# Kernel optimization log

Measured on AMD Instinct MI355X. Metric: run time of the kernel, lower is better.

Reference implementation:

```python
import jax, jax.numpy as jnp
import numpy as np

NUM_GROUPS = 17
NUM_OCCLUDED = 10
TEMP = 0.1


def setup_inputs() -> dict:
    key = jax.random.key(0)
    k1, k2 = jax.random.split(key)
    B, N, D = 128, 577, 768
    x = jax.random.normal(k1, (B, N, D), dtype=jnp.float32)
    # xavier_uniform-like scale for (D, G) weight
    bound = float(np.sqrt(6.0 / (D + NUM_GROUPS)))
    group_weights = jax.random.uniform(k2, (D, NUM_GROUPS), dtype=jnp.float32, minval=-bound, maxval=bound)
    return {"x": x, "group_weights": group_weights}


def _l2_normalize(v):
    # matches F.normalize(dim=-1, eps=1e-12)
    return v / jnp.maximum(jnp.linalg.norm(v, axis=-1, keepdims=True), 1e-12)


def reference(x, group_weights):
    B, N, D = x.shape
    cls_token = x[:, 0, :]            # (B, D)
    patch_tokens = x[:, 1:, :]        # (B, P, D), P = N-1

    # cosine similarity of each patch with cls token
    sim = jnp.einsum('bpd,bd->bp', _l2_normalize(patch_tokens), _l2_normalize(cls_token))  # (B, P)

    # k least-similar patches are "occluded" -> zero them out
    _, occ_idx = jax.lax.top_k(-sim, NUM_OCCLUDED)  # (B, K)
    mask = jnp.ones_like(sim).at[jnp.arange(B)[:, None], occ_idx].set(0.0)  # (B, P)
    non_occ = patch_tokens * mask[..., None]  # (B, P, D)

    # attention-style group pooling; softmax over groups (dim=1)
    scores = jnp.einsum('dg,bpd->bgp', group_weights, non_occ) / TEMP  # (B, G, P)
    attn = jax.nn.softmax(scores, axis=1)
    group_features = jnp.einsum('bgp,bpd->bgd', attn, non_occ)  # (B, G, D)

    # pack [global_feat, group_feat_1..G] as (B, 1+G, D)
    feats = jnp.concatenate([cls_token[:, None, :], group_features], axis=1)
    return feats, attn
```

## Files before the change

### kernel.cpp

```cpp
#include <hip/hip_runtime.h>
#include <math.h>

#define B_ 128
#define NTOK 577
#define P_ 576
#define D_ 768
#define G_ 17
#define KOCC 10
#define INV_TEMP 10.0f
#define U17 (1.0f / 17.0f)

#define OFF_WT 0
#define OFF_SIM (G_ * D_)
#define OFF_CLSINV (OFF_SIM + B_ * P_)
#define OFF_OCC (OFF_CLSINV + B_)
#define OFF_GFP (OFF_OCC + B_ * KOCC)
#define GFP_PART ((size_t)B_ * G_ * D_)

__global__ __launch_bounds__(256) void k0_cls(const float* __restrict__ x,
                                              const float* __restrict__ gw,
                                              float* __restrict__ feats,
                                              float* __restrict__ clsinv,
                                              float* __restrict__ wt,
                                              int zero_groups) {
    if (blockIdx.x >= B_) {
        int g = blockIdx.x - B_;
        for (int d = threadIdx.x; d < D_; d += 256)
            wt[g * D_ + d] = gw[d * G_ + g];
        return;
    }
    int b = blockIdx.x;
    const float* cls = x + (size_t)b * NTOK * D_;
    float* fb = feats + (size_t)b * 18 * D_;
    float ss = 0.f;
    for (int i = threadIdx.x; i < D_ / 4; i += 256) {
        float4 v = ((const float4*)cls)[i];
        ((float4*)fb)[i] = v;
        ss = fmaf(v.x, v.x, fmaf(v.y, v.y, fmaf(v.z, v.z, fmaf(v.w, v.w, ss))));
    }
    if (zero_groups) {
        float4 z = {0.f, 0.f, 0.f, 0.f};
        for (int i = threadIdx.x; i < G_ * D_ / 4; i += 256)
            ((float4*)(fb + D_))[i] = z;
    }
    #pragma unroll
    for (int off = 32; off; off >>= 1) ss += __shfl_xor(ss, off, 64);
    __shared__ float red[4];
    int wave = threadIdx.x >> 6, lane = threadIdx.x & 63;
    if (lane == 0) red[wave] = ss;
    __syncthreads();
    if (threadIdx.x == 0) {
        float t = red[0] + red[1] + red[2] + red[3];
        clsinv[b] = 1.0f / fmaxf(sqrtf(t), 1e-12f);
    }
}

__global__ __launch_bounds__(256) void k1_score(const float* __restrict__ x,
                                                const float* __restrict__ wt,
                                                const float* __restrict__ clsinv,
                                                float* __restrict__ sim,
                                                float* __restrict__ attn) {
    __shared__ __align__(16) float buf[2][18 * 64];
    __shared__ __align__(16) float atile[19 * 68];
    int tid = threadIdx.x;
    int b = blockIdx.y, chunk = blockIdx.x;
    const float* clsrow = x + (size_t)b * NTOK * D_;

    for (int i = tid; i < 288; i += 256) {
        int r = i >> 4, c = i & 15;
        const float* src = (r < 17) ? (wt + r * D_ + c * 4) : (clsrow + c * 4);
        *(float4*)&buf[0][r * 64 + c * 4] = *(const float4*)src;
    }
    int lane = tid & 63, wave = tid >> 6;
    int lr = lane & 15, row4 = lane >> 4;
    int pbase = wave * 16 + row4 * 4;
    const float* xp0 = x + ((size_t)(b * NTOK + 1 + chunk * 64 + pbase)) * D_ + lr * 4;

    float4 xv[4], xn[4];
    #pragma unroll
    for (int m = 0; m < 4; ++m) xv[m] = *(const float4*)(xp0 + (size_t)m * D_);

    float s[19][4];
    #pragma unroll
    for (int i = 0; i < 19; ++i)
        #pragma unroll
        for (int m = 0; m < 4; ++m) s[i][m] = 0.f;
    __syncthreads();

    for (int kc = 0; kc < 12; ++kc) {
        int cb = kc & 1, nb = cb ^ 1;
        if (kc < 11) {
            #pragma unroll
            for (int m = 0; m < 4; ++m)
                xn[m] = *(const float4*)(xp0 + (kc + 1) * 64 + (size_t)m * D_);
            for (int i = tid; i < 288; i += 256) {
                int r = i >> 4, c = i & 15;
                const float* src = (r < 17) ? (wt + r * D_ + (kc + 1) * 64 + c * 4)
                                            : (clsrow + (kc + 1) * 64 + c * 4);
                *(float4*)&buf[nb][r * 64 + c * 4] = *(const float4*)src;
            }
        }
        #pragma unroll
        for (int g = 0; g < 18; ++g) {
            float4 w4 = *(const float4*)&buf[cb][g * 64 + lr * 4];
            #pragma unroll
            for (int m = 0; m < 4; ++m)
                s[g][m] = fmaf(xv[m].x, w4.x, fmaf(xv[m].y, w4.y,
                          fmaf(xv[m].z, w4.z, fmaf(xv[m].w, w4.w, s[g][m]))));
        }
        #pragma unroll
        for (int m = 0; m < 4; ++m)
            s[18][m] = fmaf(xv[m].x, xv[m].x, fmaf(xv[m].y, xv[m].y,
                       fmaf(xv[m].z, xv[m].z, fmaf(xv[m].w, xv[m].w, s[18][m]))));
        #pragma unroll
        for (int m = 0; m < 4; ++m) xv[m] = xn[m];
        __syncthreads();
    }

    #pragma unroll
    for (int off = 8; off >= 1; off >>= 1)
        #pragma unroll
        for (int i = 0; i < 19; ++i)
            #pragma unroll
            for (int m = 0; m < 4; ++m)
                s[i][m] += __shfl_xor(s[i][m], off, 16);

    #pragma unroll
    for (int g = 0; g < 19; ++g) {
        if (lr == ((g < 16) ? g : 15)) {
            float4 v = {s[g][0], s[g][1], s[g][2], s[g][3]};
            *(float4*)&atile[g * 68 + pbase] = v;
        }
    }
    __syncthreads();

    if (tid < 64) {
        int p = chunk * 64 + tid;
        float v[17];
        float mx = -3.0e38f;
        #pragma unroll
        for (int g = 0; g < 17; ++g) {
            v[g] = atile[g * 68 + tid];
            mx = fmaxf(mx, v[g]);
        }
        float tot = 0.f;
        #pragma unroll
        for (int g = 0; g < 17; ++g) {
            v[g] = __expf((v[g] - mx) * INV_TEMP);
            tot += v[g];
        }
        float inv = 1.0f / tot;
        float* ap = attn + ((size_t)b * G_) * P_ + p;
        #pragma unroll
        for (int g = 0; g < 17; ++g) ap[(size_t)g * P_] = v[g] * inv;
        float cd = atile[17 * 68 + tid];
        float sq = atile[18 * 68 + tid];
        sim[(size_t)b * P_ + p] = cd * clsinv[b] / fmaxf(sqrtf(sq), 1e-12f);
    }
}

__global__ __launch_bounds__(64) void k2_occl(const float* __restrict__ sim,
                                              float* __restrict__ attn,
                                              int* __restrict__ occ_idx) {
    int b = blockIdx.x, lane = threadIdx.x;
    int base = lane * 9;
    float v[9];
    #pragma unroll
    for (int j = 0; j < 9; ++j) v[j] = sim[(size_t)b * P_ + base + j];
    int wins[KOCC];
    for (int t = 0; t < KOCC; ++t) {
        float mv = 3.0e38f;
        int mi = 1 << 30;
        #pragma unroll
        for (int j = 0; j < 9; ++j) {
            if (v[j] < mv) { mv = v[j]; mi = base + j; }
        }
        #pragma unroll
        for (int off = 1; off < 64; off <<= 1) {
            float ov = __shfl_xor(mv, off, 64);
            int oi = __shfl_xor(mi, off, 64);
            if (ov < mv || (ov == mv && oi < mi)) { mv = ov; mi = oi; }
        }
        wins[t] = mi;
        int loc = mi - base;
        if (loc >= 0 && loc < 9) v[loc] = 3.0e38f;
    }
    if (lane == 0) {
        #pragma unroll
        for (int t = 0; t < KOCC; ++t) occ_idx[b * KOCC + t] = wins[t];
    }
    #pragma unroll
    for (int t = 0; t < KOCC; ++t) {
        if (lane < G_) attn[((size_t)b * G_ + lane) * P_ + wins[t]] = U17;
    }
}

__global__ __launch_bounds__(192) void k3_part(const float* __restrict__ x,
                                               const float* __restrict__ attn,
                                               float* __restrict__ gfp,
                                               int ppp) {
    extern __shared__ float am[];
    int tid = threadIdx.x;
    int pc = blockIdx.x, b = blockIdx.y;
    int p0 = pc * ppp;

    for (int i = tid; i < G_ * ppp; i += 192) {
        int g = i / ppp;
        int pp = i - g * ppp;
        am[i] = attn[((size_t)b * G_ + g) * P_ + p0 + pp];
    }
    __syncthreads();

    const float* xb = x + ((size_t)(b * NTOK) + 1 + p0) * D_ + tid * 4;
    float4 acc[G_];
    #pragma unroll
    for (int g = 0; g < G_; ++g) acc[g] = make_float4(0.f, 0.f, 0.f, 0.f);

    float4 c0 = *(const float4*)(xb + (size_t)0 * D_);
    float4 c1 = *(const float4*)(xb + (size_t)1 * D_);
    float4 c2 = *(const float4*)(xb + (size_t)2 * D_);
    float4 c3 = *(const float4*)(xb + (size_t)3 * D_);

    for (int pp = 0; pp < ppp; pp += 4) {
        float4 n0, n1, n2, n3;
        if (pp + 4 < ppp) {
            n0 = *(const float4*)(xb + (size_t)(pp + 4) * D_);
            n1 = *(const float4*)(xb + (size_t)(pp + 5) * D_);
            n2 = *(const float4*)(xb + (size_t)(pp + 6) * D_);
            n3 = *(const float4*)(xb + (size_t)(pp + 7) * D_);
        }
        #pragma unroll
        for (int g = 0; g < G_; ++g) {
            float4 a = *(const float4*)&am[g * ppp + pp];
            acc[g].x = fmaf(a.x, c0.x, fmaf(a.y, c1.x, fmaf(a.z, c2.x, fmaf(a.w, c3.x, acc[g].x))));
            acc[g].y = fmaf(a.x, c0.y, fmaf(a.y, c1.y, fmaf(a.z, c2.y, fmaf(a.w, c3.y, acc[g].y))));
            acc[g].z = fmaf(a.x, c0.z, fmaf(a.y, c1.z, fmaf(a.z, c2.z, fmaf(a.w, c3.z, acc[g].z))));
            acc[g].w = fmaf(a.x, c0.w, fmaf(a.y, c1.w, fmaf(a.z, c2.w, fmaf(a.w, c3.w, acc[g].w))));
        }
        c0 = n0; c1 = n1; c2 = n2; c3 = n3;
    }

    float* gb = gfp + ((size_t)(pc * B_ + b) * G_) * D_ + tid * 4;
    #pragma unroll
    for (int g = 0; g < G_; ++g) *(float4*)(gb + (size_t)g * D_) = acc[g];
}

#define PC_ 96
__global__ __launch_bounds__(192) void k3_atomic(const float* __restrict__ x,
                                                 const float* __restrict__ attn,
                                                 float* __restrict__ feats) {
    __shared__ __align__(16) float am[G_ * PC_];
    int tid = threadIdx.x;
    int pc = blockIdx.x, b = blockIdx.y;
    int p0 = pc * PC_;
    for (int i = tid; i < G_ * PC_; i += 192) {
        int g = i / PC_;
        int pp = i - g * PC_;
        am[i] = attn[((size_t)b * G_ + g) * P_ + p0 + pp];
    }
    __syncthreads();
    const float* xb = x + ((size_t)(b * NTOK) + 1 + p0) * D_ + tid * 4;
    float4 acc[G_];
    #pragma unroll
    for (int g = 0; g < G_; ++g) acc[g] = make_float4(0.f, 0.f, 0.f, 0.f);
    for (int pp = 0; pp < PC_; pp += 4) {
        float4 x0 = *(const float4*)(xb + (size_t)(pp + 0) * D_);
        float4 x1 = *(const float4*)(xb + (size_t)(pp + 1) * D_);
        float4 x2 = *(const float4*)(xb + (size_t)(pp + 2) * D_);
        float4 x3 = *(const float4*)(xb + (size_t)(pp + 3) * D_);
        #pragma unroll
        for (int g = 0; g < G_; ++g) {
            float4 a = *(const float4*)&am[g * PC_ + pp];
            acc[g].x = fmaf(a.x, x0.x, fmaf(a.y, x1.x, fmaf(a.z, x2.x, fmaf(a.w, x3.x, acc[g].x))));
            acc[g].y = fmaf(a.x, x0.y, fmaf(a.y, x1.y, fmaf(a.z, x2.y, fmaf(a.w, x3.y, acc[g].y))));
            acc[g].z = fmaf(a.x, x0.z, fmaf(a.y, x1.z, fmaf(a.z, x2.z, fmaf(a.w, x3.z, acc[g].z))));
            acc[g].w = fmaf(a.x, x0.w, fmaf(a.y, x1.w, fmaf(a.z, x2.w, fmaf(a.w, x3.w, acc[g].w))));
        }
    }
    float* fb = feats + ((size_t)(b * 18) + 1) * D_ + tid * 4;
    #pragma unroll
    for (int g = 0; g < G_; ++g) {
        atomicAdd(fb + (size_t)g * D_ + 0, acc[g].x);
        atomicAdd(fb + (size_t)g * D_ + 1, acc[g].y);
        atomicAdd(fb + (size_t)g * D_ + 2, acc[g].z);
        atomicAdd(fb + (size_t)g * D_ + 3, acc[g].w);
    }
}

__global__ __launch_bounds__(192) void k4_fin(const float* __restrict__ x,
                                              const int* __restrict__ occ_idx,
                                              const float* __restrict__ gfp,
                                              int nparts,
                                              float* __restrict__ feats) {
    int b = blockIdx.x, tid = threadIdx.x;
    float* fb = feats + ((size_t)(b * 18) + 1) * D_ + tid * 4;
    float4 acc[G_];
    if (nparts == 0) {
        #pragma unroll
        for (int g = 0; g < G_; ++g) acc[g] = *(const float4*)(fb + (size_t)g * D_);
    } else {
        #pragma unroll
        for (int g = 0; g < G_; ++g) acc[g] = make_float4(0.f, 0.f, 0.f, 0.f);
        for (int pc = 0; pc < nparts; ++pc) {
            const float* gb = gfp + ((size_t)(pc * B_ + b) * G_) * D_ + tid * 4;
            #pragma unroll
            for (int g = 0; g < G_; ++g) {
                float4 v = *(const float4*)(gb + (size_t)g * D_);
                acc[g].x += v.x; acc[g].y += v.y; acc[g].z += v.z; acc[g].w += v.w;
            }
        }
    }
    float4 corr = make_float4(0.f, 0.f, 0.f, 0.f);
    for (int t = 0; t < KOCC; ++t) {
        int p = occ_idx[b * KOCC + t];
        float4 xo = *(const float4*)(x + ((size_t)(b * NTOK) + 1 + p) * D_ + tid * 4);
        corr.x += xo.x; corr.y += xo.y; corr.z += xo.z; corr.w += xo.w;
    }
    corr.x *= U17; corr.y *= U17; corr.z *= U17; corr.w *= U17;
    #pragma unroll
    for (int g = 0; g < G_; ++g) {
        float4 v = acc[g];
        v.x -= corr.x; v.y -= corr.y; v.z -= corr.z; v.w -= corr.w;
        *(float4*)(fb + (size_t)g * D_) = v;
    }
}

extern "C" void kernel_launch(void* const* d_in, const int* in_sizes, int n_in,
                              void* d_out, int out_size, void* d_ws, size_t ws_size,
                              hipStream_t stream) {
    const float* x  = (const float*)d_in[0];
    const float* gw = (const float*)d_in[1];
    float* feats = (float*)d_out;
    float* attn  = (float*)d_out + (size_t)B_ * 18 * D_;
    float* wt      = (float*)d_ws + OFF_WT;
    float* sim     = (float*)d_ws + OFF_SIM;
    float* clsinv  = (float*)d_ws + OFF_CLSINV;
    int*   occ_idx = (int*)((float*)d_ws + OFF_OCC);
    float* gfp     = (float*)d_ws + OFF_GFP;

    int nparts = 0;
    for (int n = 4; n >= 1; n >>= 1) {
        if ((OFF_GFP + (size_t)n * GFP_PART) * 4 <= ws_size) { nparts = n; break; }
    }

    k0_cls<<<B_ + G_, 256, 0, stream>>>(x, gw, feats, clsinv, wt, nparts == 0);
    k1_score<<<dim3(9, B_), 256, 0, stream>>>(x, wt, clsinv, sim, attn);
    k2_occl<<<B_, 64, 0, stream>>>(sim, attn, occ_idx);
    if (nparts > 0) {
        int ppp = P_ / nparts;
        k3_part<<<dim3(nparts, B_), 192, G_ * ppp * 4, stream>>>(x, attn, gfp, ppp);
    } else {
        k3_atomic<<<dim3(P_ / PC_, B_), 192, 0, stream>>>(x, attn, feats);
    }
    k4_fin<<<B_, 192, 0, stream>>>(x, occ_idx, gfp, nparts, feats);
}
```

Measured before the change: 412.5 us.

## Fuse score and group pooling per chunk, apply occlusion as post-hoc correction

The score kernel now keeps each 64-patch chunk's softmax attention in shared memory and immediately does the attention-weighted pooling over the same x rows, writing per-chunk partials (or atomics). Top-k occlusion selection moves into the final reduction kernel, which patches attn to uniform and subtracts each occluded patch's original contribution. This is meant to avoid a second full read of x and the separate attn round trip, and it cuts the launch count from five to three. In exchange it needs nine partial buffers in workspace and a longer k1 kernel. Masked patches first contribute with their unmasked attention and are then subtracted, so the result can differ slightly in rounding.

Result: no change. 406.5 us (-1.5%).

```diff
diff --git a/kernel.cpp b/kernel.cpp
--- a/kernel.cpp
+++ b/kernel.cpp
@@ -9,12 +9,12 @@
 #define KOCC 10
 #define INV_TEMP 10.0f
 #define U17 (1.0f / 17.0f)
+#define NCHUNK 9
 
 #define OFF_WT 0
 #define OFF_SIM (G_ * D_)
 #define OFF_CLSINV (OFF_SIM + B_ * P_)
-#define OFF_OCC (OFF_CLSINV + B_)
-#define OFF_GFP (OFF_OCC + B_ * KOCC)
+#define OFF_GFP (OFF_CLSINV + B_)
 #define GFP_PART ((size_t)B_ * G_ * D_)
 
 __global__ __launch_bounds__(256) void k0_cls(const float* __restrict__ x,
@@ -55,11 +55,14 @@
     }
 }
 
-__global__ __launch_bounds__(256) void k1_score(const float* __restrict__ x,
-                                                const float* __restrict__ wt,
-                                                const float* __restrict__ clsinv,
-                                                float* __restrict__ sim,
-                                                float* __restrict__ attn) {
+__global__ __launch_bounds__(256) void k13_score_pv(const float* __restrict__ x,
+                                                    const float* __restrict__ wt,
+                                                    const float* __restrict__ clsinv,
+                                                    float* __restrict__ sim,
+                                                    float* __restrict__ attn,
+                                                    float* __restrict__ gfp,
+                                                    float* __restrict__ feats,
+                                                    int use_part) {
     __shared__ __align__(16) float buf[2][18 * 64];
     __shared__ __align__(16) float atile[19 * 68];
     int tid = threadIdx.x;
@@ -152,66 +155,19 @@
         float inv = 1.0f / tot;
         float* ap = attn + ((size_t)b * G_) * P_ + p;
         #pragma unroll
-        for (int g = 0; g < 17; ++g) ap[(size_t)g * P_] = v[g] * inv;
+        for (int g = 0; g < 17; ++g) {
+            float av = v[g] * inv;
+            ap[(size_t)g * P_] = av;
+            atile[g * 68 + tid] = av;
+        }
         float cd = atile[17 * 68 + tid];
         float sq = atile[18 * 68 + tid];
         sim[(size_t)b * P_ + p] = cd * clsinv[b] / fmaxf(sqrtf(sq), 1e-12f);
     }
-}
-
-__global__ __launch_bounds__(64) void k2_occl(const float* __restrict__ sim,
-                                              float* __restrict__ attn,
-                                              int* __restrict__ occ_idx) {
-    int b = blockIdx.x, lane = threadIdx.x;
-    int base = lane * 9;
-    float v[9];
-    #pragma unroll
-    for (int j = 0; j < 9; ++j) v[j] = sim[(size_t)b * P_ + base + j];
-    int wins[KOCC];
-    for (int t = 0; t < KOCC; ++t) {
-        float mv = 3.0e38f;
-        int mi = 1 << 30;
-        #pragma unroll
-        for (int j = 0; j < 9; ++j) {
-            if (v[j] < mv) { mv = v[j]; mi = base + j; }
-        }
-        #pragma unroll
-        for (int off = 1; off < 64; off <<= 1) {
-            float ov = __shfl_xor(mv, off, 64);
-            int oi = __shfl_xor(mi, off, 64);
-            if (ov < mv || (ov == mv && oi < mi)) { mv = ov; mi = oi; }
-        }
-        wins[t] = mi;
-        int loc = mi - base;
-        if (loc >= 0 && loc < 9) v[loc] = 3.0e38f;
-    }
-    if (lane == 0) {
-        #pragma unroll
-        for (int t = 0; t < KOCC; ++t) occ_idx[b * KOCC + t] = wins[t];
-    }
-    #pragma unroll
-    for (int t = 0; t < KOCC; ++t) {
-        if (lane < G_) attn[((size_t)b * G_ + lane) * P_ + wins[t]] = U17;
-    }
-}
-
-__global__ __launch_bounds__(192) void k3_part(const float* __restrict__ x,
-                                               const float* __restrict__ attn,
-                                               float* __restrict__ gfp,
-                                               int ppp) {
-    extern __shared__ float am[];
-    int tid = threadIdx.x;
-    int pc = blockIdx.x, b = blockIdx.y;
-    int p0 = pc * ppp;
-
-    for (int i = tid; i < G_ * ppp; i += 192) {
-        int g = i / ppp;
-        int pp = i - g * ppp;
-        am[i] = attn[((size_t)b * G_ + g) * P_ + p0 + pp];
-    }
-    __syncthreads();
-
-    const float* xb = x + ((size_t)(b * NTOK) + 1 + p0) * D_ + tid * 4;
+    __syncthreads();
+
+    if (tid >= 192) return;
+    const float* xb = x + ((size_t)(b * NTOK) + 1 + chunk * 64) * D_ + tid * 4;
     float4 acc[G_];
     #pragma unroll
     for (int g = 0; g < G_; ++g) acc[g] = make_float4(0.f, 0.f, 0.f, 0.f);
@@ -221,9 +177,9 @@
     float4 c2 = *(const float4*)(xb + (size_t)2 * D_);
     float4 c3 = *(const float4*)(xb + (size_t)3 * D_);
 
-    for (int pp = 0; pp < ppp; pp += 4) {
-        float4 n0, n1, n2, n3;
-        if (pp + 4 < ppp) {
+    for (int pp = 0; pp < 64; pp += 4) {
+        float4 n0 = c0, n1 = c1, n2 = c2, n3 = c3;
+        if (pp + 4 < 64) {
             n0 = *(const float4*)(xb + (size_t)(pp + 4) * D_);
             n1 = *(const float4*)(xb + (size_t)(pp + 5) * D_);
             n2 = *(const float4*)(xb + (size_t)(pp + 6) * D_);
@@ -231,7 +187,7 @@
         }
         #pragma unroll
         for (int g = 0; g < G_; ++g) {
-            float4 a = *(const float4*)&am[g * ppp + pp];
+            float4 a = *(const float4*)&atile[g * 68 + pp];
             acc[g].x = fmaf(a.x, c0.x, fmaf(a.y, c1.x, fmaf(a.z, c2.x, fmaf(a.w, c3.x, acc[g].x))));
             acc[g].y = fmaf(a.x, c0.y, fmaf(a.y, c1.y, fmaf(a.z, c2.y, fmaf(a.w, c3.y, acc[g].y))));
             acc[g].z = fmaf(a.x, c0.z, fmaf(a.y, c1.z, fmaf(a.z, c2.z, fmaf(a.w, c3.z, acc[g].z))));
@@ -240,68 +196,63 @@
         c0 = n0; c1 = n1; c2 = n2; c3 = n3;
     }
 
-    float* gb = gfp + ((size_t)(pc * B_ + b) * G_) * D_ + tid * 4;
-    #pragma unroll
-    for (int g = 0; g < G_; ++g) *(float4*)(gb + (size_t)g * D_) = acc[g];
+    if (use_part) {
+        float* gb = gfp + ((size_t)(chunk * B_ + b) * G_) * D_ + tid * 4;
+        #pragma unroll
+        for (int g = 0; g < G_; ++g) *(float4*)(gb + (size_t)g * D_) = acc[g];
+    } else {
+        float* fb = feats + ((size_t)(b * 18) + 1) * D_ + tid * 4;
+        #pragma unroll
+        for (int g = 0; g < G_; ++g) {
+            atomicAdd(fb + (size_t)g * D_ + 0, acc[g].x);
+            atomicAdd(fb + (size_t)g * D_ + 1, acc[g].y);
+            atomicAdd(fb + (size_t)g * D_ + 2, acc[g].z);
+            atomicAdd(fb + (size_t)g * D_ + 3, acc[g].w);
+        }
+    }
 }
 
-#define PC_ 96
-__global__ __launch_bounds__(192) void k3_atomic(const float* __restrict__ x,
-                                                 const float* __restrict__ attn,
-                                                 float* __restrict__ feats) {
-    __shared__ __align__(16) float am[G_ * PC_];
-    int tid = threadIdx.x;
-    int pc = blockIdx.x, b = blockIdx.y;
-    int p0 = pc * PC_;
-    for (int i = tid; i < G_ * PC_; i += 192) {
-        int g = i / PC_;
-        int pp = i - g * PC_;
-        am[i] = attn[((size_t)b * G_ + g) * P_ + p0 + pp];
-    }
-    __syncthreads();
-    const float* xb = x + ((size_t)(b * NTOK) + 1 + p0) * D_ + tid * 4;
+__global__ __launch_bounds__(192) void k24_fin(const float* __restrict__ x,
+                                               const float* __restrict__ sim,
+                                               const float* __restrict__ gfp,
+                                               float* __restrict__ attn,
+                                               float* __restrict__ feats,
+                                               int use_part) {
+    __shared__ int s_occ[KOCC];
+    __shared__ float s_a0[KOCC][G_];
+    int b = blockIdx.x, tid = threadIdx.x;
+
+    if (tid < 64) {
+        int lane = tid;
+        int base = lane * 9;
+        float v[9];
+        #pragma unroll
+        for (int j = 0; j < 9; ++j) v[j] = sim[(size_t)b * P_ + base + j];
+        for (int t = 0; t < KOCC; ++t) {
+            float mv = 3.0e38f;
+            int mi = 1 << 30;
+            #pragma unroll
+            for (int j = 0; j < 9; ++j) {
+                if (v[j] < mv) { mv = v[j]; mi = base + j; }
+            }
+            #pragma unroll
+            for (int off = 1; off < 64; off <<= 1) {
+                float ov = __shfl_xor(mv, off, 64);
+                int oi = __shfl_xor(mi, off, 64);
+                if (ov < mv || (ov == mv && oi < mi)) { mv = ov; mi = oi; }
+            }
+            if (lane == 0) s_occ[t] = mi;
+            int loc = mi - base;
+            if (loc >= 0 && loc < 9) v[loc] = 3.0e38f;
+        }
+    }
+
     float4 acc[G_];
-    #pragma unroll
-    for (int g = 0; g < G_; ++g) acc[g] = make_float4(0.f, 0.f, 0.f, 0.f);
-    for (int pp = 0; pp < PC_; pp += 4) {
-        float4 x0 = *(const float4*)(xb + (size_t)(pp + 0) * D_);
-        float4 x1 = *(const float4*)(xb + (size_t)(pp + 1) * D_);
-        float4 x2 = *(const float4*)(xb + (size_t)(pp + 2) * D_);
-        float4 x3 = *(const float4*)(xb + (size_t)(pp + 3) * D_);
-        #pragma unroll
-        for (int g = 0; g < G_; ++g) {
-            float4 a = *(const float4*)&am[g * PC_ + pp];
-            acc[g].x = fmaf(a.x, x0.x, fmaf(a.y, x1.x, fmaf(a.z, x2.x, fmaf(a.w, x3.x, acc[g].x))));
-            acc[g].y = fmaf(a.x, x0.y, fmaf(a.y, x1.y, fmaf(a.z, x2.y, fmaf(a.w, x3.y, acc[g].y))));
-            acc[g].z = fmaf(a.x, x0.z, fmaf(a.y, x1.z, fmaf(a.z, x2.z, fmaf(a.w, x3.z, acc[g].z))));
-            acc[g].w = fmaf(a.x, x0.w, fmaf(a.y, x1.w, fmaf(a.z, x2.w, fmaf(a.w, x3.w, acc[g].w))));
-        }
-    }
     float* fb = feats + ((size_t)(b * 18) + 1) * D_ + tid * 4;
-    #pragma unroll
-    for (int g = 0; g < G_; ++g) {
-        atomicAdd(fb + (size_t)g * D_ + 0, acc[g].x);
-        atomicAdd(fb + (size_t)g * D_ + 1, acc[g].y);
-        atomicAdd(fb + (size_t)g * D_ + 2, acc[g].z);
-        atomicAdd(fb + (size_t)g * D_ + 3, acc[g].w);
-    }
-}
-
-__global__ __launch_bounds__(192) void k4_fin(const float* __restrict__ x,
-                                              const int* __restrict__ occ_idx,
-                                              const float* __restrict__ gfp,
-                                              int nparts,
-                                              float* __restrict__ feats) {
-    int b = blockIdx.x, tid = threadIdx.x;
-    float* fb = feats + ((size_t)(b * 18) + 1) * D_ + tid * 4;
-    float4 acc[G_];
-    if (nparts == 0) {
-        #pragma unroll
-        for (int g = 0; g < G_; ++g) acc[g] = *(const float4*)(fb + (size_t)g * D_);
-    } else {
+    if (use_part) {
         #pragma unroll
         for (int g = 0; g < G_; ++g) acc[g] = make_float4(0.f, 0.f, 0.f, 0.f);
-        for (int pc = 0; pc < nparts; ++pc) {
+        for (int pc = 0; pc < NCHUNK; ++pc) {
             const float* gb = gfp + ((size_t)(pc * B_ + b) * G_) * D_ + tid * 4;
             #pragma unroll
             for (int g = 0; g < G_; ++g) {
@@ -309,20 +260,34 @@
                 acc[g].x += v.x; acc[g].y += v.y; acc[g].z += v.z; acc[g].w += v.w;
             }
         }
-    }
-    float4 corr = make_float4(0.f, 0.f, 0.f, 0.f);
+    } else {
+        #pragma unroll
+        for (int g = 0; g < G_; ++g) acc[g] = *(const float4*)(fb + (size_t)g * D_);
+    }
+    __syncthreads();
+
+    for (int i = tid; i < KOCC * G_; i += 192) {
+        int t = i / G_, g = i - t * G_;
+        size_t idx = ((size_t)b * G_ + g) * P_ + s_occ[t];
+        s_a0[t][g] = attn[idx];
+        attn[idx] = U17;
+    }
+    __syncthreads();
+
+    #pragma unroll
     for (int t = 0; t < KOCC; ++t) {
-        int p = occ_idx[b * KOCC + t];
-        float4 xo = *(const float4*)(x + ((size_t)(b * NTOK) + 1 + p) * D_ + tid * 4);
-        corr.x += xo.x; corr.y += xo.y; corr.z += xo.z; corr.w += xo.w;
-    }
-    corr.x *= U17; corr.y *= U17; corr.z *= U17; corr.w *= U17;
-    #pragma unroll
-    for (int g = 0; g < G_; ++g) {
-        float4 v = acc[g];
-        v.x -= corr.x; v.y -= corr.y; v.z -= corr.z; v.w -= corr.w;
-        *(float4*)(fb + (size_t)g * D_) = v;
-    }
+        float4 xo = *(const float4*)(x + ((size_t)(b * NTOK) + 1 + s_occ[t]) * D_ + tid * 4);
+        #pragma unroll
+        for (int g = 0; g < G_; ++g) {
+            float a0 = s_a0[t][g];
+            acc[g].x = fmaf(-a0, xo.x, acc[g].x);
+            acc[g].y = fmaf(-a0, xo.y, acc[g].y);
+            acc[g].z = fmaf(-a0, xo.z, acc[g].z);
+            acc[g].w = fmaf(-a0, xo.w, acc[g].w);
+        }
+    }
+    #pragma unroll
+    for (int g = 0; g < G_; ++g) *(float4*)(fb + (size_t)g * D_) = acc[g];
 }
 
 extern "C" void kernel_launch(void* const* d_in, const int* in_sizes, int n_in,
@@ -335,22 +300,11 @@
     float* wt      = (float*)d_ws + OFF_WT;
     float* sim     = (float*)d_ws + OFF_SIM;
     float* clsinv  = (float*)d_ws + OFF_CLSINV;
-    int*   occ_idx = (int*)((float*)d_ws + OFF_OCC);
     float* gfp     = (float*)d_ws + OFF_GFP;
 
-    int nparts = 0;
-    for (int n = 4; n >= 1; n >>= 1) {
-        if ((OFF_GFP + (size_t)n * GFP_PART) * 4 <= ws_size) { nparts = n; break; }
-    }
-
-    k0_cls<<<B_ + G_, 256, 0, stream>>>(x, gw, feats, clsinv, wt, nparts == 0);
-    k1_score<<<dim3(9, B_), 256, 0, stream>>>(x, wt, clsinv, sim, attn);
-    k2_occl<<<B_, 64, 0, stream>>>(sim, attn, occ_idx);
-    if (nparts > 0) {
-        int ppp = P_ / nparts;
-        k3_part<<<dim3(nparts, B_), 192, G_ * ppp * 4, stream>>>(x, attn, gfp, ppp);
-    } else {
-        k3_atomic<<<dim3(P_ / PC_, B_), 192, 0, stream>>>(x, attn, feats);
-    }
-    k4_fin<<<B_, 192, 0, stream>>>(x, occ_idx, gfp, nparts, feats);
+    int use_part = (((size_t)OFF_GFP + (size_t)NCHUNK * GFP_PART) * sizeof(float) <= ws_size);
+
+    k0_cls<<<B_ + G_, 256, 0, stream>>>(x, gw, feats, clsinv, wt, !use_part);
+    k13_score_pv<<<dim3(NCHUNK, B_), 256, 0, stream>>>(x, wt, clsinv, sim, attn, gfp, feats, use_part);
+    k24_fin<<<B_, 192, 0, stream>>>(x, sim, gfp, attn, feats, use_part);
 }
```
